# Optimization experiments

Measured on AMD Instinct MI355X. Metric: run time of the kernel, lower is better.

The kernel has to match this reference:

```python
import jax, jax.numpy as jnp
import numpy as np

B, C, D, J = 8, 2048, 128, 128

def setup_inputs() -> dict:
    key = jax.random.key(0)
    ks = jax.random.split(key, 24)
    s = 0.02
    inp = {
        "operation_features": jax.random.normal(ks[0], (B, C, D), jnp.float32),
        "relations": jax.random.randint(ks[1], (B, C - 2, 2), 0, C, jnp.int64),
        "begins_idx": jax.random.randint(ks[2], (B, J), 0, C, jnp.int64),
        "ends_idx": jax.random.randint(ks[3], (B, J), 0, C, jnp.int64),
        "same_type_mask": (jax.random.uniform(ks[4], (B, C, C)) > 0.5).astype(jnp.float32),
        # BeginEndEncoder
        "W_begin": jax.random.normal(ks[5], (D, D), jnp.float32) * s,
        "b_begin": jnp.zeros((D,), jnp.float32),
        "W_end": jax.random.normal(ks[6], (D, D), jnp.float32) * s,
        "b_end": jnp.zeros((D,), jnp.float32),
        # OperationTimeRelationEncoder.mix: Linear(3D -> D)
        "W_mix3": jax.random.normal(ks[7], (3 * D, D), jnp.float32) * s,
        "b_mix3": jnp.zeros((D,), jnp.float32),
        # SelfAttention (hidden_dim = D)
        "W_qkv": jax.random.normal(ks[8], (D, 3 * D), jnp.float32) * s,
        "b_qkv": jnp.zeros((3 * D,), jnp.float32),
        "w_score": jax.random.normal(ks[9], (2 * D,), jnp.float32) * s,
        "b_score": jnp.zeros((), jnp.float32),
        "W_out": jax.random.normal(ks[10], (D, D), jnp.float32) * s,
        "b_out": jnp.zeros((D,), jnp.float32),
        # block mix: Linear(2D -> D)
        "W_mix2": jax.random.normal(ks[11], (2 * D, D), jnp.float32) * s,
        "b_mix2": jnp.zeros((D,), jnp.float32),
    }
    return inp

def _gather_ops(ops, idx):
    # ops: [B,C,D], idx: [B,M] -> [B,M,D]  (torch.gather along dim 1 with expanded index)
    Bb, _, Dd = ops.shape
    M = idx.shape[1]
    return jnp.take_along_axis(ops, jnp.broadcast_to(idx[:, :, None], (Bb, M, Dd)), axis=1)

def reference(operation_features, relations, begins_idx, ends_idx, same_type_mask,
              W_begin, b_begin, W_end, b_end, W_mix3, b_mix3,
              W_qkv, b_qkv, w_score, b_score, W_out, b_out, W_mix2, b_mix2):
    ops = operation_features
    Dd = ops.shape[-1]
    # --- OperationTimeRelationEncoder ---
    pred = _gather_ops(ops, relations[..., 0])      # [B,C-2,D]
    succ = _gather_ops(ops, relations[..., 1])      # [B,C-2,D]
    concated = jnp.concatenate([ops[:, :-2, :], pred, succ], axis=-1)  # [B,C-2,3D]
    mixed = concated @ W_mix3 + b_mix3              # [B,C-2,D]
    begin_f = _gather_ops(ops, begins_idx) @ W_begin + b_begin  # [B,J,D]
    end_f = _gather_ops(ops, ends_idx) @ W_end + b_end
    begin = jnp.mean(begin_f, axis=1)               # [B,D]
    end = jnp.mean(end_f, axis=1)
    seq = jnp.concatenate([mixed, begin[:, None, :], end[:, None, :]], axis=1)  # [B,C,D]
    # --- SelfAttention (GAT-style additive score, decomposed to avoid CxCx2h blowup) ---
    qkv = ops @ W_qkv + b_qkv                       # [B,C,3D]
    q, k, v = jnp.split(qkv, 3, axis=-1)
    sq = q @ w_score[:Dd]                           # [B,C]  q_i . w_q
    sk = k @ w_score[Dd:]                           # [B,C]  k_j . w_k
    scores = jax.nn.leaky_relu(sq[:, :, None] + sk[:, None, :] + b_score)  # [B,C,C]
    attn = jax.nn.softmax(scores * same_type_mask, axis=-1)                # multiplicative mask, as in torch
    weighted = jnp.einsum('bij,bjd->bid', attn, v)  # [B,C,D]
    same_type = weighted @ W_out + b_out            # [B,C,D]
    # --- final mix ---
    return jnp.concatenate([seq, same_type], axis=-1) @ W_mix2 + b_mix2  # [B,C,D]
```

## Files before the change

kernel.cpp:

```cpp
#include <hip/hip_runtime.h>
#include <cstddef>

typedef __bf16 bf16;
typedef __bf16 bf16x4 __attribute__((ext_vector_type(4)));
typedef __bf16 bf16x8 __attribute__((ext_vector_type(8)));
typedef float  f32x4  __attribute__((ext_vector_type(4)));

#define MFMA16(a, b, c) __builtin_amdgcn_mfma_f32_16x16x32_bf16((a), (b), (c), 0, 0, 0)

#define BB 8
#define CC 2048
#define DD 128
#define JJN 128

#define WS_VT    ((size_t)0)
#define WS_OATT  ((size_t)4194304)
#define WS_OPS16 ((size_t)8388608)
#define WS_SQF   ((size_t)12582912)
#define WS_SKF   ((size_t)12648448)
#define WS_G1T   ((size_t)12713984)
#define WS_G2T   ((size_t)12746752)
#define WS_G3T   ((size_t)12779520)
#define WS_WCT   ((size_t)12812288)
#define WS_GBT   ((size_t)12845056)
#define WS_GET   ((size_t)12877824)
#define WS_UQK   ((size_t)12910592)
#define WS_BBM   ((size_t)12911104)
#define WS_BBB   ((size_t)12911616)
#define WS_BBE   ((size_t)12912128)
#define WS_SC    ((size_t)12912640)

__global__ __launch_bounds__(256) void k_prepcast(
    const float* __restrict__ ops, bf16* __restrict__ ops16,
    const float* __restrict__ Wmix3, const float* __restrict__ Wmix2,
    const float* __restrict__ Wout,  const float* __restrict__ Wbegin,
    const float* __restrict__ Wend,  const float* __restrict__ Wqkv,
    const float* __restrict__ bqkv,  const float* __restrict__ wscore,
    const float* __restrict__ bscore,const float* __restrict__ bmix3,
    const float* __restrict__ bout,  const float* __restrict__ bmix2,
    const float* __restrict__ bbegin,const float* __restrict__ bend,
    bf16* __restrict__ G1T, bf16* __restrict__ G2T, bf16* __restrict__ G3T,
    bf16* __restrict__ WCT, bf16* __restrict__ GBT, bf16* __restrict__ GET,
    bf16* __restrict__ uqk, float* __restrict__ BBM, float* __restrict__ BBB,
    float* __restrict__ BBE, float* __restrict__ sc)
{
    __shared__ bf16  LshT[128 * 132];
    __shared__ float Rsh[128 * 8];
    int wg = blockIdx.x;
    int t  = threadIdx.x;

    if (wg < 1024) {
        size_t i = (size_t)wg * 256 + t;
        f32x4 a = *(const f32x4*)(ops + i * 8);
        f32x4 b = *(const f32x4*)(ops + i * 8 + 4);
        bf16x8 o;
        #pragma unroll
        for (int e = 0; e < 4; ++e) { o[e] = (bf16)a[e]; o[4 + e] = (bf16)b[e]; }
        *(bf16x8*)(ops16 + i * 8) = o;
        return;
    }
    if (wg < 1120) {
        int id  = wg - 1024;
        int mat = id >> 4, sub = id & 15;
        const float* L; const float* R; bf16* O;
        switch (mat) {
            case 0: L = Wmix3;           R = Wmix2;           O = G1T; break;
            case 1: L = Wmix3 + 128*128; R = Wmix2;           O = G2T; break;
            case 2: L = Wmix3 + 256*128; R = Wmix2;           O = G3T; break;
            case 3: L = Wout;            R = Wmix2 + 128*128; O = WCT; break;
            case 4: L = Wbegin;          R = Wmix2;           O = GBT; break;
            default:L = Wend;            R = Wmix2;           O = GET; break;
        }
        int e0 = sub * 8;
        #pragma unroll
        for (int pass = 0; pass < 16; ++pass) {
            int idx = pass * 256 + t;
            int d   = idx >> 5;
            int f0  = (idx & 31) * 4;
            f32x4 v = *(const f32x4*)(L + d * 128 + f0);
            #pragma unroll
            for (int jj = 0; jj < 4; ++jj)
                LshT[(f0 + jj) * 132 + d] = (bf16)v[jj];
        }
        #pragma unroll
        for (int pass = 0; pass < 4; ++pass) {
            int idx = pass * 256 + t;
            int f   = idx >> 3;
            int ee  = idx & 7;
            Rsh[f * 8 + ee] = R[f * 128 + e0 + ee];
        }
        __syncthreads();
        int ee = t >> 5;
        int e  = e0 + ee;
        int d0 = (t & 31) * 4;
        float s[4] = {0.f, 0.f, 0.f, 0.f};
        for (int f = 0; f < 128; ++f) {
            bf16x4 lv = *(const bf16x4*)&LshT[f * 132 + d0];
            float rv = Rsh[f * 8 + ee];
            #pragma unroll
            for (int dd = 0; dd < 4; ++dd)
                s[dd] += (float)lv[dd] * rv;
        }
        #pragma unroll
        for (int dd = 0; dd < 4; ++dd)
            O[e * 128 + d0 + dd] = (bf16)s[dd];
        return;
    }
    if (t < 128) {
        int d = t;
        float su = 0.f, sk_ = 0.f;
        for (int e2 = 0; e2 < 128; ++e2) {
            su  += Wqkv[d*384 + e2]       * wscore[e2];
            sk_ += Wqkv[d*384 + 128 + e2] * wscore[128 + e2];
        }
        uqk[d]       = (bf16)su;
        uqk[128 + d] = (bf16)sk_;
        int e = d;
        float bm = 0.f, bon = 0.f, bb_ = 0.f, be_ = 0.f;
        for (int f = 0; f < 128; ++f) {
            float w2a = Wmix2[f*128 + e];
            float w2b = Wmix2[(128+f)*128 + e];
            bm  += bmix3[f]  * w2a;
            bon += bout[f]   * w2b;
            bb_ += bbegin[f] * w2a;
            be_ += bend[f]   * w2a;
        }
        float bm2 = bmix2[e];
        BBM[e] = bm  + bon + bm2;
        BBB[e] = bb_ + bon + bm2;
        BBE[e] = be_ + bon + bm2;
    } else if (t == 128) {
        float cq = 0.f, ck = 0.f;
        for (int e2 = 0; e2 < 128; ++e2) {
            cq += bqkv[e2]       * wscore[e2];
            ck += bqkv[128 + e2] * wscore[128 + e2];
        }
        sc[0] = cq + bscore[0];
        sc[1] = ck;
    }
}

__global__ __launch_bounds__(256) void k_v(
    const bf16* __restrict__ ops16, const float* __restrict__ Wqkv,
    const float* __restrict__ bqkv, const bf16* __restrict__ uqk,
    const float* __restrict__ sc,
    bf16* __restrict__ VT, float* __restrict__ sqf, float* __restrict__ skf)
{
    __shared__ bf16 A[144 * 136];
    int b  = blockIdx.x >> 4;
    int jt = (blockIdx.x & 15) * 128;
    int t  = threadIdx.x;
    #pragma unroll
    for (int pass = 0; pass < 16; ++pass) {
        int idx = pass * 256 + t;
        int d   = idx >> 5;
        int n0  = (idx & 31) * 4;
        f32x4 v = *(const f32x4*)(Wqkv + d*384 + 256 + n0);
        #pragma unroll
        for (int jj = 0; jj < 4; ++jj)
            A[(n0 + jj)*136 + d] = (bf16)v[jj];
    }
    {
        int row = t >> 7, col = t & 127;
        A[(128 + row)*136 + col] = uqk[row*128 + col];
    }
    for (int idx = t; idx < 14*136; idx += 256)
        A[130*136 + idx] = (bf16)0.f;
    __syncthreads();

    int lane = t & 63, w = t >> 6;
    int m = lane & 15, q = lane >> 4;
    f32x4 acc[9][2];
    #pragma unroll
    for (int rb = 0; rb < 9; ++rb)
        #pragma unroll
        for (int cb = 0; cb < 2; ++cb)
            acc[rb][cb] = {0.f, 0.f, 0.f, 0.f};

    const bf16* opsb = ops16 + (size_t)b * CC * DD;
    #pragma unroll
    for (int kc = 0; kc < 4; ++kc) {
        bf16x8 bfr[2];
        #pragma unroll
        for (int cb = 0; cb < 2; ++cb) {
            int j = jt + w*32 + cb*16 + m;
            bfr[cb] = *(const bf16x8*)(opsb + (size_t)j*DD + kc*32 + q*8);
        }
        #pragma unroll
        for (int rb = 0; rb < 9; ++rb) {
            bf16x8 afr = *(const bf16x8*)&A[(rb*16 + m)*136 + kc*32 + q*8];
            acc[rb][0] = MFMA16(afr, bfr[0], acc[rb][0]);
            acc[rb][1] = MFMA16(afr, bfr[1], acc[rb][1]);
        }
    }
    float cqb = sc[0], ckv = sc[1];
    #pragma unroll
    for (int cb = 0; cb < 2; ++cb) {
        int j = jt + w*32 + cb*16 + m;
        #pragma unroll
        for (int rb = 0; rb < 8; ++rb) {
            #pragma unroll
            for (int r = 0; r < 4; ++r) {
                int n = rb*16 + q*4 + r;
                float v = acc[rb][cb][r] + bqkv[256 + n];
                VT[((size_t)b*DD + n)*CC + j] = (bf16)v;
            }
        }
        if (q == 0) {
            sqf[b*CC + j] = acc[8][cb][0] + cqb;
            skf[b*CC + j] = acc[8][cb][1] + ckv;
        }
    }
}

struct AttBuf { f32x4 mk0, mk1, s0, s1; bf16x8 vb[8]; };

__device__ __forceinline__ void att_load(int jc, int q, int m,
    const float* __restrict__ maskrow, const float* __restrict__ skrow,
    const bf16* __restrict__ vtb, AttBuf& Bu)
{
    int jj = jc*32 + q*8;
    Bu.mk0 = __builtin_nontemporal_load((const f32x4*)(maskrow + jj));
    Bu.mk1 = __builtin_nontemporal_load((const f32x4*)(maskrow + jj + 4));
    Bu.s0 = *(const f32x4*)(skrow + jj);
    Bu.s1 = *(const f32x4*)(skrow + jj + 4);
    #pragma unroll
    for (int nb = 0; nb < 8; ++nb)
        Bu.vb[nb] = *(const bf16x8*)(vtb + ((size_t)(nb*16 + m))*CC + jj);
}

__device__ __forceinline__ void att_step(const AttBuf& Bu, float sq,
                                         float& lsum, f32x4 acc[8])
{
    float sks[8] = {Bu.s0[0], Bu.s0[1], Bu.s0[2], Bu.s0[3],
                    Bu.s1[0], Bu.s1[1], Bu.s1[2], Bu.s1[3]};
    float mks[8] = {Bu.mk0[0], Bu.mk0[1], Bu.mk0[2], Bu.mk0[3],
                    Bu.mk1[0], Bu.mk1[1], Bu.mk1[2], Bu.mk1[3]};
    bf16x8 a;
    #pragma unroll
    for (int e = 0; e < 8; ++e) {
        float tv = sq + sks[e];
        float lr = fmaxf(tv, 0.01f * tv);
        float z  = lr * mks[e];
        float p  = __expf(z);
        lsum += p;
        a[e] = (bf16)p;
    }
    #pragma unroll
    for (int nb = 0; nb < 8; ++nb)
        acc[nb] = MFMA16(a, Bu.vb[nb], acc[nb]);
}

__global__ __launch_bounds__(256) void k_att(
    const float* __restrict__ mask, const bf16* __restrict__ VT,
    const float* __restrict__ sqf, const float* __restrict__ skf,
    bf16* __restrict__ Oatt)
{
    __shared__ float Osh[4 * 16 * 132];
    __shared__ float Lsh[4 * 16];
    int t    = threadIdx.x;
    int lane = t & 63;
    int w    = t >> 6;
    int tile = blockIdx.x;
    int b    = tile >> 7;
    int i0   = (tile & 127) << 4;
    int m = lane & 15, q = lane >> 4;
    int i = i0 + m;

    float sq = sqf[b*CC + i];
    f32x4 acc[8];
    #pragma unroll
    for (int nb = 0; nb < 8; ++nb) acc[nb] = {0.f, 0.f, 0.f, 0.f};
    float lsum = 0.f;

    const float* maskrow = mask + ((size_t)(b*CC + i)) * CC;
    const float* skrow   = skf + b*CC;
    const bf16*  vtb     = VT + (size_t)b * DD * CC;

    int jc0 = w * 16;
    AttBuf bufA, bufB;
    att_load(jc0, q, m, maskrow, skrow, vtb, bufA);
    for (int s = 0; s < 16; s += 2) {
        att_load(jc0 + s + 1, q, m, maskrow, skrow, vtb, bufB);
        att_step(bufA, sq, lsum, acc);
        if (s + 2 < 16) att_load(jc0 + s + 2, q, m, maskrow, skrow, vtb, bufA);
        att_step(bufB, sq, lsum, acc);
    }

    lsum += __shfl_xor(lsum, 16, 64);
    lsum += __shfl_xor(lsum, 32, 64);
    if (q == 0) Lsh[w*16 + m] = lsum;
    #pragma unroll
    for (int nb = 0; nb < 8; ++nb)
        #pragma unroll
        for (int r = 0; r < 4; ++r)
            Osh[(w*16 + q*4 + r)*132 + nb*16 + m] = acc[nb][r];
    __syncthreads();

    int r  = t >> 4;
    int c0 = (t & 15) * 8;
    float l = Lsh[r] + Lsh[16 + r] + Lsh[32 + r] + Lsh[48 + r];
    float inv = 1.0f / l;
    bf16x8 o;
    #pragma unroll
    for (int e = 0; e < 8; ++e) {
        float s = Osh[(r)*132 + c0 + e] + Osh[(16 + r)*132 + c0 + e]
                + Osh[(32 + r)*132 + c0 + e] + Osh[(48 + r)*132 + c0 + e];
        o[e] = (bf16)(s * inv);
    }
    *(bf16x8*)(Oatt + ((size_t)(b*CC) + i0 + r)*DD + c0) = o;
}

__global__ __launch_bounds__(256) void k_epi(
    const bf16* __restrict__ ops16, const int* __restrict__ relations,
    const bf16* __restrict__ Oatt,
    const bf16* __restrict__ G1T, const bf16* __restrict__ G2T,
    const bf16* __restrict__ G3T, const bf16* __restrict__ WCT,
    const float* __restrict__ BBM, float* __restrict__ out)
{
    __shared__ bf16 Abuf[64 * 136];
    __shared__ bf16 Bbuf[128 * 136];
    int b  = blockIdx.x >> 5;
    int c0 = (blockIdx.x & 31) * 64;
    int t  = threadIdx.x;
    int lane = t & 63, w = t >> 6;
    int m = lane & 15, q = lane >> 4;

    f32x4 acc[4][2];
    #pragma unroll
    for (int rb = 0; rb < 4; ++rb)
        #pragma unroll
        for (int cb = 0; cb < 2; ++cb)
            acc[rb][cb] = {0.f, 0.f, 0.f, 0.f};

    const bf16* Bsrc[4] = {G1T, G2T, G3T, WCT};
    int arow = t >> 2, aq = t & 3;
    int brow = t >> 1, bhalf = t & 1;
    int c = c0 + arow;

    for (int term = 0; term < 4; ++term) {
        const bf16* src;
        if (term == 0)      src = ops16 + ((size_t)(b*CC + c)) * DD;
        else if (term == 3) src = Oatt  + ((size_t)(b*CC + c)) * DD;
        else {
            int cc = min(c, CC - 3);
            int ridx = relations[((size_t)b*(CC-2) + cc)*2 + (term - 1)];
            src = ops16 + ((size_t)(b*CC) + ridx) * DD;
        }
        const uint4* s4 = (const uint4*)(src + aq*32);
        uint4* d4 = (uint4*)&Abuf[arow*136 + aq*32];
        #pragma unroll
        for (int ii = 0; ii < 4; ++ii) d4[ii] = s4[ii];

        const uint4* bs = (const uint4*)(Bsrc[term] + brow*128 + bhalf*64);
        uint4* bd = (uint4*)&Bbuf[brow*136 + bhalf*64];
        #pragma unroll
        for (int ii = 0; ii < 8; ++ii) bd[ii] = bs[ii];
        __syncthreads();

        #pragma unroll
        for (int kc = 0; kc < 4; ++kc) {
            bf16x8 bfr[2];
            #pragma unroll
            for (int cb = 0; cb < 2; ++cb)
                bfr[cb] = *(const bf16x8*)&Bbuf[(w*32 + cb*16 + m)*136 + kc*32 + q*8];
            #pragma unroll
            for (int rb = 0; rb < 4; ++rb) {
                bf16x8 afr = *(const bf16x8*)&Abuf[(rb*16 + m)*136 + kc*32 + q*8];
                acc[rb][0] = MFMA16(afr, bfr[0], acc[rb][0]);
                acc[rb][1] = MFMA16(afr, bfr[1], acc[rb][1]);
            }
        }
        __syncthreads();
    }
    #pragma unroll
    for (int cb = 0; cb < 2; ++cb) {
        int col = w*32 + cb*16 + m;
        float bias = BBM[col];
        #pragma unroll
        for (int rb = 0; rb < 4; ++rb) {
            #pragma unroll
            for (int r = 0; r < 4; ++r) {
                int cg = c0 + rb*16 + q*4 + r;
                if (cg < CC - 2)
                    out[((size_t)(b*CC) + cg)*DD + col] = acc[rb][cb][r] + bias;
            }
        }
    }
}

__global__ __launch_bounds__(128) void k_edge(
    const bf16* __restrict__ ops16, const int* __restrict__ begins,
    const int* __restrict__ ends, const bf16* __restrict__ Oatt,
    const bf16* __restrict__ GBT, const bf16* __restrict__ GET,
    const bf16* __restrict__ WCT, const float* __restrict__ BBB,
    const float* __restrict__ BBE, float* __restrict__ out)
{
    __shared__ float meanv[128];
    int b = blockIdx.x >> 1, which = blockIdx.x & 1;
    int t = threadIdx.x;
    const int* idx = which ? (ends + b*JJN) : (begins + b*JJN);
    const bf16* opsb = ops16 + (size_t)b * CC * DD;
    float s = 0.f;
    for (int j = 0; j < JJN; ++j) {
        int r = idx[j];
        s += (float)opsb[(size_t)r*DD + t];
    }
    meanv[t] = s * (1.0f / (float)JJN);
    __syncthreads();
    const bf16* G  = which ? GET : GBT;
    const float* Bv = which ? BBE : BBB;
    const bf16* orow = Oatt + ((size_t)b*CC + (CC - 2 + which)) * DD;
    float a = Bv[t];
    const bf16* gr = G + t*128;
    const bf16* wr = WCT + t*128;
    for (int d = 0; d < 128; ++d) {
        a += meanv[d] * (float)gr[d];
        a += (float)orow[d] * (float)wr[d];
    }
    out[((size_t)b*CC + (CC - 2 + which))*DD + t] = a;
}

extern "C" void kernel_launch(void* const* d_in, const int* in_sizes, int n_in,
                              void* d_out, int out_size, void* d_ws, size_t ws_size,
                              hipStream_t stream)
{
    const float* ops      = (const float*)d_in[0];
    const int*  relations = (const int*)d_in[1];
    const int*  begins    = (const int*)d_in[2];
    const int*  ends      = (const int*)d_in[3];
    const float* mask     = (const float*)d_in[4];
    const float* Wbegin   = (const float*)d_in[5];
    const float* bbegin   = (const float*)d_in[6];
    const float* Wend     = (const float*)d_in[7];
    const float* bend     = (const float*)d_in[8];
    const float* Wmix3    = (const float*)d_in[9];
    const float* bmix3    = (const float*)d_in[10];
    const float* Wqkv     = (const float*)d_in[11];
    const float* bqkv     = (const float*)d_in[12];
    const float* wscore   = (const float*)d_in[13];
    const float* bscore   = (const float*)d_in[14];
    const float* Wout     = (const float*)d_in[15];
    const float* bout     = (const float*)d_in[16];
    const float* Wmix2    = (const float*)d_in[17];
    const float* bmix2    = (const float*)d_in[18];
    float* outp = (float*)d_out;

    char* ws = (char*)d_ws;
    bf16*  VT    = (bf16*)(ws + WS_VT);
    bf16*  Oatt  = (bf16*)(ws + WS_OATT);
    bf16*  OPS16 = (bf16*)(ws + WS_OPS16);
    float* sqf   = (float*)(ws + WS_SQF);
    float* skf   = (float*)(ws + WS_SKF);
    bf16*  G1T   = (bf16*)(ws + WS_G1T);
    bf16*  G2T   = (bf16*)(ws + WS_G2T);
    bf16*  G3T   = (bf16*)(ws + WS_G3T);
    bf16*  WCT   = (bf16*)(ws + WS_WCT);
    bf16*  GBT   = (bf16*)(ws + WS_GBT);
    bf16*  GET   = (bf16*)(ws + WS_GET);
    bf16*  UQK   = (bf16*)(ws + WS_UQK);
    float* BBM   = (float*)(ws + WS_BBM);
    float* BBB   = (float*)(ws + WS_BBB);
    float* BBE   = (float*)(ws + WS_BBE);
    float* SC    = (float*)(ws + WS_SC);

    k_prepcast<<<dim3(1121), dim3(256), 0, stream>>>(
        ops, OPS16,
        Wmix3, Wmix2, Wout, Wbegin, Wend, Wqkv, bqkv, wscore, bscore,
        bmix3, bout, bmix2, bbegin, bend,
        G1T, G2T, G3T, WCT, GBT, GET, UQK, BBM, BBB, BBE, SC);

    k_v<<<dim3(128), dim3(256), 0, stream>>>(
        OPS16, Wqkv, bqkv, UQK, SC, VT, sqf, skf);

    k_att<<<dim3(1024), dim3(256), 0, stream>>>(
        mask, VT, sqf, skf, Oatt);

    k_epi<<<dim3(256), dim3(256), 0, stream>>>(
        OPS16, relations, Oatt, G1T, G2T, G3T, WCT, BBM, outp);

    k_edge<<<dim3(16), dim3(128), 0, stream>>>(
        OPS16, begins, ends, Oatt, GBT, GET, WCT, BBB, BBE, outp);
}
```

Before: 339.8 us.

## Pack V in MFMA fragment layout, stage mask via LDS, retile epilogue

V is now written in a packed layout that matches the MFMA B-fragment order, so each fragment load in the attention kernel is a contiguous 16-byte read rather than a strided access across the transposed V. Mask rows are loaded coalesced across 16 rows, converted to bf16, and double-buffered in LDS per wave. The sk scores are cached in LDS, and blocks are interleaved across batches by block index. The epilogue kernel moves to 32-row tiles with twice as many blocks to raise occupancy, at the cost of reloading the weight tiles more often.

```diff
diff --git a/kernel.cpp b/kernel.cpp
--- a/kernel.cpp
+++ b/kernel.cpp
@@ -13,7 +13,7 @@
 #define DD 128
 #define JJN 128
 
-#define WS_VT    ((size_t)0)
+#define WS_PK    ((size_t)0)
 #define WS_OATT  ((size_t)4194304)
 #define WS_OPS16 ((size_t)8388608)
 #define WS_SQF   ((size_t)12582912)
@@ -144,7 +144,7 @@
     const bf16* __restrict__ ops16, const float* __restrict__ Wqkv,
     const float* __restrict__ bqkv, const bf16* __restrict__ uqk,
     const float* __restrict__ sc,
-    bf16* __restrict__ VT, float* __restrict__ sqf, float* __restrict__ skf)
+    bf16* __restrict__ PK, float* __restrict__ sqf, float* __restrict__ skf)
 {
     __shared__ bf16 A[144 * 136];
     int b  = blockIdx.x >> 4;
@@ -194,16 +194,18 @@
         }
     }
     float cqb = sc[0], ckv = sc[1];
+    bf16* pkb = PK + (size_t)b * DD * CC;
     #pragma unroll
     for (int cb = 0; cb < 2; ++cb) {
-        int j = jt + w*32 + cb*16 + m;
+        int j  = jt + w*32 + cb*16 + m;
+        int jc = j >> 5, jl = j & 31;
+        int qq = jl >> 3, e = jl & 7;
         #pragma unroll
         for (int rb = 0; rb < 8; ++rb) {
             #pragma unroll
             for (int r = 0; r < 4; ++r) {
-                int n = rb*16 + q*4 + r;
-                float v = acc[rb][cb][r] + bqkv[256 + n];
-                VT[((size_t)b*DD + n)*CC + j] = (bf16)v;
+                float v = acc[rb][cb][r] + bqkv[256 + rb*16 + q*4 + r];
+                pkb[((size_t)(((jc*8 + rb)*4 + qq)*16 + (q*4 + r)))*8 + e] = (bf16)v;
             }
         }
         if (q == 0) {
@@ -213,80 +215,117 @@
     }
 }
 
-struct AttBuf { f32x4 mk0, mk1, s0, s1; bf16x8 vb[8]; };
-
-__device__ __forceinline__ void att_load(int jc, int q, int m,
-    const float* __restrict__ maskrow, const float* __restrict__ skrow,
-    const bf16* __restrict__ vtb, AttBuf& Bu)
-{
-    int jj = jc*32 + q*8;
-    Bu.mk0 = __builtin_nontemporal_load((const f32x4*)(maskrow + jj));
-    Bu.mk1 = __builtin_nontemporal_load((const f32x4*)(maskrow + jj + 4));
-    Bu.s0 = *(const f32x4*)(skrow + jj);
-    Bu.s1 = *(const f32x4*)(skrow + jj + 4);
+struct MaskLd { f32x4 v[4]; };
+
+__device__ __forceinline__ MaskLd stage_load(const float* __restrict__ mrow0,
+                                             int st, int lane)
+{
+    MaskLd L;
+    int rr0 = lane >> 4, cc = (lane & 15) * 4;
+    const float* src = mrow0 + st * 64 + cc;
+    #pragma unroll
+    for (int k = 0; k < 4; ++k)
+        L.v[k] = __builtin_nontemporal_load(
+            (const f32x4*)(src + ((size_t)(rr0 + k * 4)) * CC));
+    return L;
+}
+
+__device__ __forceinline__ void stage_write(const MaskLd& L, bf16* mb,
+                                            int st, int lane)
+{
+    int rr0 = lane >> 4, cc = (lane & 15) * 4;
+    bf16* dst = mb + (st & 1) * 1152;
+    #pragma unroll
+    for (int k = 0; k < 4; ++k) {
+        bf16x4 o;
+        #pragma unroll
+        for (int e = 0; e < 4; ++e) o[e] = (bf16)L.v[k][e];
+        *(bf16x4*)(dst + (rr0 + k * 4) * 72 + cc) = o;
+    }
+}
+
+__device__ __forceinline__ void load_vb(const bf16* __restrict__ pkb, int jc,
+                                        int q, int m, bf16x8 vb[8])
+{
     #pragma unroll
     for (int nb = 0; nb < 8; ++nb)
-        Bu.vb[nb] = *(const bf16x8*)(vtb + ((size_t)(nb*16 + m))*CC + jj);
-}
-
-__device__ __forceinline__ void att_step(const AttBuf& Bu, float sq,
-                                         float& lsum, f32x4 acc[8])
-{
-    float sks[8] = {Bu.s0[0], Bu.s0[1], Bu.s0[2], Bu.s0[3],
-                    Bu.s1[0], Bu.s1[1], Bu.s1[2], Bu.s1[3]};
-    float mks[8] = {Bu.mk0[0], Bu.mk0[1], Bu.mk0[2], Bu.mk0[3],
-                    Bu.mk1[0], Bu.mk1[1], Bu.mk1[2], Bu.mk1[3]};
+        vb[nb] = *(const bf16x8*)(pkb + ((size_t)(((jc*8 + nb)*4 + q)*16 + m)) * 8);
+}
+
+__device__ __forceinline__ void substep(const bf16* mb, const float* skb,
+    int st, int sub, int q, int m, float sq, const bf16x8 vb[8],
+    float& lsum, f32x4 acc[8])
+{
+    bf16x8 mk = *(const bf16x8*)(mb + (st & 1) * 1152 + m * 72 + sub * 32 + q * 8);
+    int jo = st * 64 + sub * 32 + q * 8;
+    f32x4 s0 = *(const f32x4*)(skb + jo);
+    f32x4 s1 = *(const f32x4*)(skb + jo + 4);
+    float sks[8] = {s0[0], s0[1], s0[2], s0[3], s1[0], s1[1], s1[2], s1[3]};
     bf16x8 a;
     #pragma unroll
     for (int e = 0; e < 8; ++e) {
         float tv = sq + sks[e];
         float lr = fmaxf(tv, 0.01f * tv);
-        float z  = lr * mks[e];
+        float z  = lr * (float)mk[e];
         float p  = __expf(z);
         lsum += p;
         a[e] = (bf16)p;
     }
     #pragma unroll
     for (int nb = 0; nb < 8; ++nb)
-        acc[nb] = MFMA16(a, Bu.vb[nb], acc[nb]);
-}
-
-__global__ __launch_bounds__(256) void k_att(
-    const float* __restrict__ mask, const bf16* __restrict__ VT,
+        acc[nb] = MFMA16(a, vb[nb], acc[nb]);
+}
+
+__global__ __launch_bounds__(256, 3) void k_att(
+    const float* __restrict__ mask, const bf16* __restrict__ PK,
     const float* __restrict__ sqf, const float* __restrict__ skf,
     bf16* __restrict__ Oatt)
 {
-    __shared__ float Osh[4 * 16 * 132];
-    __shared__ float Lsh[4 * 16];
+    __shared__ __align__(16) char smem[34048];
     int t    = threadIdx.x;
-    int lane = t & 63;
-    int w    = t >> 6;
-    int tile = blockIdx.x;
-    int b    = tile >> 7;
-    int i0   = (tile & 127) << 4;
+    int lane = t & 63, w = t >> 6;
+    int b    = blockIdx.x & 7;
+    int i0   = (blockIdx.x >> 3) << 4;
     int m = lane & 15, q = lane >> 4;
-    int i = i0 + m;
-
-    float sq = sqf[b*CC + i];
+
+    bf16*  mbuf = (bf16*)(smem + w * 4608);
+    float* skb  = (float*)(smem + 18432 + w * 2048);
+
+    {
+        const float* src = skf + b*CC + w*512;
+        f32x4 v0 = *(const f32x4*)(src + lane*4);
+        f32x4 v1 = *(const f32x4*)(src + 256 + lane*4);
+        *(f32x4*)(skb + lane*4) = v0;
+        *(f32x4*)(skb + 256 + lane*4) = v1;
+    }
+    float sq = sqf[b*CC + i0 + m];
+    const float* mrow0 = mask + ((size_t)(b*CC + i0))*CC + w*512;
+    const bf16*  pkb   = PK + (size_t)b * DD * CC;
+    int jc0 = w * 16;
+
     f32x4 acc[8];
     #pragma unroll
     for (int nb = 0; nb < 8; ++nb) acc[nb] = {0.f, 0.f, 0.f, 0.f};
     float lsum = 0.f;
 
-    const float* maskrow = mask + ((size_t)(b*CC + i)) * CC;
-    const float* skrow   = skf + b*CC;
-    const bf16*  vtb     = VT + (size_t)b * DD * CC;
-
-    int jc0 = w * 16;
-    AttBuf bufA, bufB;
-    att_load(jc0, q, m, maskrow, skrow, vtb, bufA);
-    for (int s = 0; s < 16; s += 2) {
-        att_load(jc0 + s + 1, q, m, maskrow, skrow, vtb, bufB);
-        att_step(bufA, sq, lsum, acc);
-        if (s + 2 < 16) att_load(jc0 + s + 2, q, m, maskrow, skrow, vtb, bufA);
-        att_step(bufB, sq, lsum, acc);
-    }
-
+    MaskLd L0 = stage_load(mrow0, 0, lane);
+    stage_write(L0, mbuf, 0, lane);
+    bf16x8 vbA[8], vbB[8];
+    load_vb(pkb, jc0, q, m, vbA);
+
+    for (int st = 0; st < 8; ++st) {
+        MaskLd Ln;
+        if (st < 7) Ln = stage_load(mrow0, st + 1, lane);
+        load_vb(pkb, jc0 + st*2 + 1, q, m, vbB);
+        substep(mbuf, skb, st, 0, q, m, sq, vbA, lsum, acc);
+        if (st < 7) load_vb(pkb, jc0 + st*2 + 2, q, m, vbA);
+        substep(mbuf, skb, st, 1, q, m, sq, vbB, lsum, acc);
+        if (st < 7) stage_write(Ln, mbuf, st + 1, lane);
+    }
+
+    __syncthreads();
+    float* Osh = (float*)smem;
+    float* Lsh = (float*)(smem + 33792);
     lsum += __shfl_xor(lsum, 16, 64);
     lsum += __shfl_xor(lsum, 32, 64);
     if (q == 0) Lsh[w*16 + m] = lsum;
@@ -304,7 +343,7 @@
     bf16x8 o;
     #pragma unroll
     for (int e = 0; e < 8; ++e) {
-        float s = Osh[(r)*132 + c0 + e] + Osh[(16 + r)*132 + c0 + e]
+        float s = Osh[r*132 + c0 + e] + Osh[(16 + r)*132 + c0 + e]
                 + Osh[(32 + r)*132 + c0 + e] + Osh[(48 + r)*132 + c0 + e];
         o[e] = (bf16)(s * inv);
     }
@@ -318,24 +357,24 @@
     const bf16* __restrict__ G3T, const bf16* __restrict__ WCT,
     const float* __restrict__ BBM, float* __restrict__ out)
 {
-    __shared__ bf16 Abuf[64 * 136];
+    __shared__ bf16 Abuf[32 * 136];
     __shared__ bf16 Bbuf[128 * 136];
-    int b  = blockIdx.x >> 5;
-    int c0 = (blockIdx.x & 31) * 64;
+    int b  = blockIdx.x >> 6;
+    int c0 = (blockIdx.x & 63) * 32;
     int t  = threadIdx.x;
     int lane = t & 63, w = t >> 6;
     int m = lane & 15, q = lane >> 4;
 
-    f32x4 acc[4][2];
-    #pragma unroll
-    for (int rb = 0; rb < 4; ++rb)
+    f32x4 acc[2][2];
+    #pragma unroll
+    for (int rb = 0; rb < 2; ++rb)
         #pragma unroll
         for (int cb = 0; cb < 2; ++cb)
             acc[rb][cb] = {0.f, 0.f, 0.f, 0.f};
 
     const bf16* Bsrc[4] = {G1T, G2T, G3T, WCT};
-    int arow = t >> 2, aq = t & 3;
-    int brow = t >> 1, bhalf = t & 1;
+    int arow = t >> 3, ao = (t & 7) * 16;
+    int brow = t >> 1, bo = (t & 1) * 64;
     int c = c0 + arow;
 
     for (int term = 0; term < 4; ++term) {
@@ -343,17 +382,14 @@
         if (term == 0)      src = ops16 + ((size_t)(b*CC + c)) * DD;
         else if (term == 3) src = Oatt  + ((size_t)(b*CC + c)) * DD;
         else {
-            int cc = min(c, CC - 3);
-            int ridx = relations[((size_t)b*(CC-2) + cc)*2 + (term - 1)];
+            int ridx = relations[((size_t)b*(CC-2) + min(c, CC-3))*2 + (term - 1)];
             src = ops16 + ((size_t)(b*CC) + ridx) * DD;
         }
-        const uint4* s4 = (const uint4*)(src + aq*32);
-        uint4* d4 = (uint4*)&Abuf[arow*136 + aq*32];
-        #pragma unroll
-        for (int ii = 0; ii < 4; ++ii) d4[ii] = s4[ii];
-
-        const uint4* bs = (const uint4*)(Bsrc[term] + brow*128 + bhalf*64);
-        uint4* bd = (uint4*)&Bbuf[brow*136 + bhalf*64];
+        *(uint4*)&Abuf[arow*136 + ao]     = *(const uint4*)(src + ao);
+        *(uint4*)&Abuf[arow*136 + ao + 8] = *(const uint4*)(src + ao + 8);
+
+        const uint4* bs = (const uint4*)(Bsrc[term] + brow*128 + bo);
+        uint4* bd = (uint4*)&Bbuf[brow*136 + bo];
         #pragma unroll
         for (int ii = 0; ii < 8; ++ii) bd[ii] = bs[ii];
         __syncthreads();
@@ -365,7 +401,7 @@
             for (int cb = 0; cb < 2; ++cb)
                 bfr[cb] = *(const bf16x8*)&Bbuf[(w*32 + cb*16 + m)*136 + kc*32 + q*8];
             #pragma unroll
-            for (int rb = 0; rb < 4; ++rb) {
+            for (int rb = 0; rb < 2; ++rb) {
                 bf16x8 afr = *(const bf16x8*)&Abuf[(rb*16 + m)*136 + kc*32 + q*8];
                 acc[rb][0] = MFMA16(afr, bfr[0], acc[rb][0]);
                 acc[rb][1] = MFMA16(afr, bfr[1], acc[rb][1]);
@@ -378,7 +414,7 @@
         int col = w*32 + cb*16 + m;
         float bias = BBM[col];
         #pragma unroll
-        for (int rb = 0; rb < 4; ++rb) {
+        for (int rb = 0; rb < 2; ++rb) {
             #pragma unroll
             for (int r = 0; r < 4; ++r) {
                 int cg = c0 + rb*16 + q*4 + r;
@@ -447,7 +483,7 @@
     float* outp = (float*)d_out;
 
     char* ws = (char*)d_ws;
-    bf16*  VT    = (bf16*)(ws + WS_VT);
+    bf16*  PK    = (bf16*)(ws + WS_PK);
     bf16*  Oatt  = (bf16*)(ws + WS_OATT);
     bf16*  OPS16 = (bf16*)(ws + WS_OPS16);
     float* sqf   = (float*)(ws + WS_SQF);
@@ -471,12 +507,12 @@
         G1T, G2T, G3T, WCT, GBT, GET, UQK, BBM, BBB, BBE, SC);
 
     k_v<<<dim3(128), dim3(256), 0, stream>>>(
-        OPS16, Wqkv, bqkv, UQK, SC, VT, sqf, skf);
+        OPS16, Wqkv, bqkv, UQK, SC, PK, sqf, skf);
 
     k_att<<<dim3(1024), dim3(256), 0, stream>>>(
-        mask, VT, sqf, skf, Oatt);
-
-    k_epi<<<dim3(256), dim3(256), 0, stream>>>(
+        mask, PK, sqf, skf, Oatt);
+
+    k_epi<<<dim3(512), dim3(256), 0, stream>>>(
         OPS16, relations, Oatt, G1T, G2T, G3T, WCT, BBM, outp);
 
     k_edge<<<dim3(16), dim3(128), 0, stream>>>(
```

After: 313.0 us. 7.9% less time.
